# Optimization experiments

Hardware: AMD Instinct MI355X
Metric: run time of the kernel (lower is better)

Reference implementation:

```python
import jax, jax.numpy as jnp
import numpy as np

B, Q, K, D, H = 2, 2048, 2048, 1024, 16
HD = D // H  # 64
EPS = 1e-6  # flax LayerNorm default epsilon


def setup_inputs() -> dict:
    key = jax.random.key(0)
    ks = jax.random.split(key, 12)
    s = 1.0 / np.sqrt(D)  # lecun_normal-like scale
    inputs_q = jax.random.normal(ks[0], (B, Q, D), jnp.float32)
    bias = jax.random.normal(ks[1], (B, 1, Q, K), jnp.float32)
    mask = jax.random.randint(ks[2], (B, 1, Q, K), 0, 2).astype(jnp.bool_)
    wq = jax.random.normal(ks[3], (D, H, HD), jnp.float32) * s
    wk = jax.random.normal(ks[4], (D, H, HD), jnp.float32) * s
    wv = jax.random.normal(ks[5], (D, H, HD), jnp.float32) * s
    bq = jnp.zeros((H, HD), jnp.float32)
    bk = jnp.zeros((H, HD), jnp.float32)
    bv = jnp.zeros((H, HD), jnp.float32)
    q_scale = jnp.ones((HD,), jnp.float32)
    k_scale = jnp.ones((HD,), jnp.float32)
    wo = jax.random.normal(ks[6], (H, HD, D), jnp.float32) * s
    bo = jnp.zeros((D,), jnp.float32)
    return dict(inputs_q=inputs_q, bias=bias, mask=mask, wq=wq, bq=bq,
                wk=wk, bk=bk, wv=wv, bv=bv, q_scale=q_scale, k_scale=k_scale,
                wo=wo, bo=bo)


def _layernorm_nobias(x, scale):
    # normalize over last axis (head_dim), no bias, like flax LayerNorm(use_bias=False)
    mean = jnp.mean(x, axis=-1, keepdims=True)
    var = jnp.mean(jnp.square(x - mean), axis=-1, keepdims=True)
    return (x - mean) * jax.lax.rsqrt(var + EPS) * scale


def reference(inputs_q, bias, mask, wq, bq, wk, bk, wv, bv, q_scale, k_scale, wo, bo):
    # QKV projections (self-attention: k and v inputs default to inputs_q)
    q = jnp.einsum('bqd,dhe->bqhe', inputs_q, wq) + bq  # [B,Q,H,HD]
    k = jnp.einsum('bkd,dhe->bkhe', inputs_q, wk) + bk  # [B,K,H,HD]
    v = jnp.einsum('bkd,dhe->bkhe', inputs_q, wv) + bv  # [B,K,H,HD]
    # optional QK layernorm (normalize_qk=True)
    q = _layernorm_nobias(q, q_scale)
    k = _layernorm_nobias(k, k_scale)
    # attention weights
    q = q / jnp.sqrt(jnp.asarray(q.shape[-1], q.dtype))
    attn = jnp.einsum('bqhe,bkhe->bhqk', q, k)  # [B,H,Q,K]
    attn = attn + bias
    big_neg = jnp.finfo(q.dtype).min
    attn = jnp.where(mask, attn, big_neg)
    attn = jax.nn.softmax(attn.astype(jnp.float32), axis=-1).astype(q.dtype)
    # weighted values + output projection
    x = jnp.einsum('bhqk,bkhe->bqhe', attn, v)  # [B,Q,H,HD]
    out = jnp.einsum('bqhe,heo->bqo', x, wo) + bo  # [B,Q,D]
    return out
```

## Files before the change

kernel.cpp:

```cpp
#include <hip/hip_runtime.h>
#include <cstdint>
#include <cstddef>

typedef __bf16 bf16_t;
typedef __bf16 bf16x8 __attribute__((ext_vector_type(8)));
typedef float f32x4 __attribute__((ext_vector_type(4)));

constexpr int BB = 2, SS = 2048, DD = 1024, HH = 16, HDIM = 64;
constexpr int BS = BB * SS;
constexpr float LOG2E = 1.4426950408889634f;

__global__ void convert_x(const float* __restrict__ src, bf16_t* __restrict__ dst, int n4) {
  int i = blockIdx.x * blockDim.x + threadIdx.x;
  if (i >= n4) return;
  float4 v = ((const float4*)src)[i];
  union { bf16_t h[4]; uint2 u; } o;
  o.h[0] = (bf16_t)v.x; o.h[1] = (bf16_t)v.y; o.h[2] = (bf16_t)v.z; o.h[3] = (bf16_t)v.w;
  ((uint2*)dst)[i] = o.u;
}

__global__ void transpose_convert(const float* __restrict__ wq, const float* __restrict__ wk,
                                  const float* __restrict__ wv, const float* __restrict__ wo,
                                  bf16_t* __restrict__ wqkv_t, bf16_t* __restrict__ wo_t) {
  int which = blockIdx.z;
  const float* src = (which == 0) ? wq : (which == 1) ? wk : (which == 2) ? wv : wo;
  bf16_t* dst = (which < 3) ? wqkv_t : wo_t;
  int noff = (which < 3) ? which * 1024 : 0;
  __shared__ float tile[64][65];
  int tr = blockIdx.y, tc = blockIdx.x;
  int t = threadIdx.x;
#pragma unroll
  for (int p = 0; p < 4; ++p) {
    int e = (p * 256 + t) * 4;
    int r = e >> 6, c = e & 63;
    float4 v = *(const float4*)&src[(size_t)(tr * 64 + r) * 1024 + tc * 64 + c];
    tile[r][c] = v.x; tile[r][c + 1] = v.y; tile[r][c + 2] = v.z; tile[r][c + 3] = v.w;
  }
  __syncthreads();
#pragma unroll
  for (int p = 0; p < 4; ++p) {
    int e = (p * 256 + t) * 4;
    int r = e >> 6, c = e & 63;
    union { bf16_t h[4]; uint2 u; } o;
#pragma unroll
    for (int j = 0; j < 4; ++j) o.h[j] = (bf16_t)tile[c + j][r];
    *(uint2*)&dst[(size_t)(noff + tc * 64 + r) * 1024 + tr * 64 + c] = o.u;
  }
}

__global__ void prep_biasmask(const float* __restrict__ bias, const int* __restrict__ mask,
                              bf16_t* __restrict__ bmT) {
  __shared__ float tile[64][65];
  int qt = blockIdx.x, kt = blockIdx.y, b = blockIdx.z;
  int t = threadIdx.x;
  const size_t base = ((size_t)b * SS + qt * 64) * SS + kt * 64;
#pragma unroll
  for (int p = 0; p < 4; ++p) {
    int e = (p * 256 + t) * 4;
    int r = e >> 6, c = e & 63;
    float4 bv = *(const float4*)&bias[base + (size_t)r * SS + c];
    int4 mv = *(const int4*)&mask[base + (size_t)r * SS + c];
    tile[r][c]     = mv.x ? bv.x * LOG2E : -2.0e38f;
    tile[r][c + 1] = mv.y ? bv.y * LOG2E : -2.0e38f;
    tile[r][c + 2] = mv.z ? bv.z * LOG2E : -2.0e38f;
    tile[r][c + 3] = mv.w ? bv.w * LOG2E : -2.0e38f;
  }
  __syncthreads();
  const size_t obase = ((size_t)b * SS + kt * 64) * SS + qt * 64;
#pragma unroll
  for (int p = 0; p < 2; ++p) {
    int e = (p * 256 + t) * 8;
    int r = e >> 6, c = e & 63;
    union { bf16_t h[8]; uint4 u; } o;
#pragma unroll
    for (int j = 0; j < 8; ++j) o.h[j] = (bf16_t)tile[c + j][r];
    *(uint4*)&bmT[obase + (size_t)r * SS + c] = o.u;
  }
}

__global__ void vt_relayout(const bf16_t* __restrict__ Cqkv, const float* __restrict__ bv,
                            bf16_t* __restrict__ vt) {
  __shared__ float tile[64][65];
  int st = blockIdx.x, h = blockIdx.y, b = blockIdx.z;
  int t = threadIdx.x;
#pragma unroll
  for (int p = 0; p < 2; ++p) {
    int e = (p * 256 + t) * 8;
    int r = e >> 6, c = e & 63;
    bf16x8 v8 = *(const bf16x8*)&Cqkv[(size_t)(b * SS + st * 64 + r) * 3072 + 2048 + h * 64 + c];
#pragma unroll
    for (int j = 0; j < 8; ++j) tile[r][c + j] = (float)v8[j] + bv[h * 64 + c + j];
  }
  __syncthreads();
#pragma unroll
  for (int p = 0; p < 2; ++p) {
    int e = (p * 256 + t) * 8;
    int r = e >> 6, c = e & 63;
    union { bf16_t h[8]; uint4 u; } o;
#pragma unroll
    for (int j = 0; j < 8; ++j) o.h[j] = (bf16_t)tile[c + j][r];
    *(uint4*)&vt[(size_t)((b * HH + h) * HDIM + r) * SS + st * 64 + c] = o.u;
  }
}

template <bool OUT_F32>
__global__ __launch_bounds__(256) void gemm_bt(const bf16_t* __restrict__ A,
                                               const bf16_t* __restrict__ Bt,
                                               bf16_t* __restrict__ Cb, float* __restrict__ Cf,
                                               const float* __restrict__ bias, int M, int N,
                                               int Kd) {
  __shared__ __align__(16) bf16_t As[128][72];
  __shared__ __align__(16) bf16_t Bs[128][72];
  int tid = threadIdx.x;
  int lane = tid & 63, w = tid >> 6;
  int lo = lane & 15, quad = lane >> 4;
  int wm = w >> 1, wn = w & 1;
  int m0 = blockIdx.y * 128, n0 = blockIdx.x * 128;
  f32x4 acc[4][4] = {};
  for (int kk = 0; kk < Kd; kk += 64) {
#pragma unroll
    for (int p = 0; p < 4; ++p) {
      int idx = (p * 256 + tid) * 8;
      int r = idx >> 6, c = idx & 63;
      *(bf16x8*)&As[r][c] = *(const bf16x8*)&A[(size_t)(m0 + r) * Kd + kk + c];
      *(bf16x8*)&Bs[r][c] = *(const bf16x8*)&Bt[(size_t)(n0 + r) * Kd + kk + c];
    }
    __syncthreads();
#pragma unroll
    for (int kc = 0; kc < 2; ++kc) {
      bf16x8 am[4], bn[4];
#pragma unroll
      for (int i = 0; i < 4; ++i)
        am[i] = *(const bf16x8*)&As[wm * 64 + i * 16 + lo][kc * 32 + quad * 8];
#pragma unroll
      for (int i = 0; i < 4; ++i)
        bn[i] = *(const bf16x8*)&Bs[wn * 64 + i * 16 + lo][kc * 32 + quad * 8];
#pragma unroll
      for (int mi = 0; mi < 4; ++mi)
#pragma unroll
        for (int ni = 0; ni < 4; ++ni)
          acc[mi][ni] = __builtin_amdgcn_mfma_f32_16x16x32_bf16(am[mi], bn[ni], acc[mi][ni], 0, 0, 0);
    }
    __syncthreads();
  }
#pragma unroll
  for (int mi = 0; mi < 4; ++mi) {
#pragma unroll
    for (int ni = 0; ni < 4; ++ni) {
#pragma unroll
      for (int r = 0; r < 4; ++r) {
        int row = m0 + wm * 64 + mi * 16 + quad * 4 + r;
        int col = n0 + wn * 64 + ni * 16 + lo;
        float v = acc[mi][ni][r];
        if (OUT_F32)
          Cf[(size_t)row * N + col] = v + bias[col];
        else
          Cb[(size_t)row * N + col] = (bf16_t)v;
      }
    }
  }
}

__global__ void ln_relayout(const bf16_t* __restrict__ Cqkv, const float* __restrict__ bq,
                            const float* __restrict__ bk, const float* __restrict__ q_scale,
                            const float* __restrict__ k_scale, bf16_t* __restrict__ qb,
                            bf16_t* __restrict__ kb) {
  int mode = blockIdx.y;
  int vec = blockIdx.x * 4 + (threadIdx.x >> 6);
  int lane = threadIdx.x & 63;
  int bs = vec >> 4, h = vec & 15;
  int b = bs >> 11, s = bs & 2047;
  const float* badd = (mode == 0) ? bq : bk;
  float x = (float)Cqkv[(size_t)bs * 3072 + mode * 1024 + h * 64 + lane] + badd[h * 64 + lane];
  float sum = x;
#pragma unroll
  for (int off = 32; off >= 1; off >>= 1) sum += __shfl_xor(sum, off, 64);
  float mean = sum * (1.0f / 64.0f);
  float d = x - mean;
  float vs = d * d;
#pragma unroll
  for (int off = 32; off >= 1; off >>= 1) vs += __shfl_xor(vs, off, 64);
  float var = vs * (1.0f / 64.0f);
  const float* sc = (mode == 0) ? q_scale : k_scale;
  float y = d * rsqrtf(var + 1e-6f) * sc[lane];
  if (mode == 0) y *= 0.125f * LOG2E;
  bf16_t* dst = (mode == 0) ? qb : kb;
  dst[(size_t)((b * 16 + h) * 2048 + s) * 64 + lane] = (bf16_t)y;
}

__global__ __launch_bounds__(256) void attn_kernel(const bf16_t* __restrict__ qb,
                                                   const bf16_t* __restrict__ kb,
                                                   const bf16_t* __restrict__ vt,
                                                   const bf16_t* __restrict__ bmT,
                                                   bf16_t* __restrict__ xout) {
  __shared__ __align__(16) bf16_t Ks[64][72];
  __shared__ __align__(16) bf16_t Vs[64][72];
  __shared__ __align__(16) bf16_t Bm[64][72];
  __shared__ __align__(16) bf16_t Ps[4][16][72];
  int tid = threadIdx.x;
  int lane = tid & 63, w = tid >> 6;
  int lo = lane & 15, quad = lane >> 4;
  int qt = blockIdx.x, h = blockIdx.y, b = blockIdx.z;
  size_t headoff = (size_t)(b * HH + h) * SS * HDIM;
  const bf16_t* vthead = vt + headoff;
  const bf16_t* bmb = bmT + (size_t)b * SS * SS;

  const bf16_t* qptr = qb + headoff + (size_t)(qt * 64 + w * 16 + lo) * HDIM;
  bf16x8 aq0 = *(const bf16x8*)(qptr + quad * 8);
  bf16x8 aq1 = *(const bf16x8*)(qptr + 32 + quad * 8);

  bf16x8 ones;
#pragma unroll
  for (int j = 0; j < 8; ++j) ones[j] = (bf16_t)1.0f;

  f32x4 o[4] = {};
  f32x4 lacc = {};

  for (int kt = 0; kt < SS / 64; ++kt) {
#pragma unroll
    for (int p = 0; p < 2; ++p) {
      int idx = (p * 256 + tid) * 8;
      int r = idx >> 6, c = idx & 63;
      *(bf16x8*)&Ks[r][c] = *(const bf16x8*)&kb[headoff + (size_t)(kt * 64 + r) * HDIM + c];
      *(bf16x8*)&Vs[r][c] = *(const bf16x8*)&vthead[(size_t)r * SS + kt * 64 + c];
      *(bf16x8*)&Bm[r][c] = *(const bf16x8*)&bmb[(size_t)(kt * 64 + r) * SS + qt * 64 + c];
    }
    __syncthreads();

    f32x4 sc[4];
#pragma unroll
    for (int c = 0; c < 4; ++c) {
      union { bf16_t h[4]; uint2 u; } bm4;
      bm4.u = *(const uint2*)&Bm[c * 16 + lo][w * 16 + quad * 4];
#pragma unroll
      for (int r = 0; r < 4; ++r) sc[c][r] = (float)bm4.h[r];
      bf16x8 bk0 = *(const bf16x8*)&Ks[c * 16 + lo][quad * 8];
      bf16x8 bk1 = *(const bf16x8*)&Ks[c * 16 + lo][32 + quad * 8];
      sc[c] = __builtin_amdgcn_mfma_f32_16x16x32_bf16(aq0, bk0, sc[c], 0, 0, 0);
      sc[c] = __builtin_amdgcn_mfma_f32_16x16x32_bf16(aq1, bk1, sc[c], 0, 0, 0);
    }
#pragma unroll
    for (int c = 0; c < 4; ++c)
#pragma unroll
      for (int r = 0; r < 4; ++r)
        Ps[w][quad * 4 + r][c * 16 + lo] = (bf16_t)__builtin_amdgcn_exp2f(sc[c][r]);
    asm volatile("s_waitcnt lgkmcnt(0)" ::: "memory");
    bf16x8 ap0 = *(const bf16x8*)&Ps[w][lo][quad * 8];
    bf16x8 ap1 = *(const bf16x8*)&Ps[w][lo][32 + quad * 8];
    lacc = __builtin_amdgcn_mfma_f32_16x16x32_bf16(ap0, ones, lacc, 0, 0, 0);
    lacc = __builtin_amdgcn_mfma_f32_16x16x32_bf16(ap1, ones, lacc, 0, 0, 0);
#pragma unroll
    for (int t2 = 0; t2 < 4; ++t2) {
      bf16x8 bv0 = *(const bf16x8*)&Vs[t2 * 16 + lo][quad * 8];
      bf16x8 bv1 = *(const bf16x8*)&Vs[t2 * 16 + lo][32 + quad * 8];
      o[t2] = __builtin_amdgcn_mfma_f32_16x16x32_bf16(ap0, bv0, o[t2], 0, 0, 0);
      o[t2] = __builtin_amdgcn_mfma_f32_16x16x32_bf16(ap1, bv1, o[t2], 0, 0, 0);
    }
    __syncthreads();
  }
  float rl[4];
#pragma unroll
  for (int r = 0; r < 4; ++r) rl[r] = 1.0f / lacc[r];
#pragma unroll
  for (int t2 = 0; t2 < 4; ++t2) {
#pragma unroll
    for (int r = 0; r < 4; ++r) {
      int qa = qt * 64 + w * 16 + quad * 4 + r;
      xout[(size_t)(b * SS + qa) * DD + h * 64 + t2 * 16 + lo] = (bf16_t)(o[t2][r] * rl[r]);
    }
  }
}

extern "C" void kernel_launch(void* const* d_in, const int* in_sizes, int n_in, void* d_out,
                              int out_size, void* d_ws, size_t ws_size, hipStream_t stream) {
  const float* inputs_q = (const float*)d_in[0];
  const float* bias = (const float*)d_in[1];
  const int* mask = (const int*)d_in[2];
  const float* wq = (const float*)d_in[3];
  const float* bq = (const float*)d_in[4];
  const float* wk = (const float*)d_in[5];
  const float* bk = (const float*)d_in[6];
  const float* wv = (const float*)d_in[7];
  const float* bv = (const float*)d_in[8];
  const float* q_scale = (const float*)d_in[9];
  const float* k_scale = (const float*)d_in[10];
  const float* wo = (const float*)d_in[11];
  const float* bo = (const float*)d_in[12];
  float* out = (float*)d_out;

  char* ws = (char*)d_ws;
  bf16_t* xb     = (bf16_t*)(ws);
  bf16_t* wqkv_t = (bf16_t*)(ws + ((size_t)8 << 20));
  bf16_t* wo_t   = (bf16_t*)(ws + ((size_t)14 << 20));
  bf16_t* cqkv   = (bf16_t*)(ws + ((size_t)16 << 20));
  bf16_t* bmT    = (bf16_t*)(ws + ((size_t)16 << 20));
  bf16_t* qb2    = (bf16_t*)(ws + ((size_t)40 << 20));
  bf16_t* kb2    = (bf16_t*)(ws + ((size_t)48 << 20));
  bf16_t* vt     = (bf16_t*)(ws + ((size_t)56 << 20));
  bf16_t* xattn  = (bf16_t*)(ws + ((size_t)64 << 20));

  convert_x<<<(BS * DD / 4 + 255) / 256, 256, 0, stream>>>(inputs_q, xb, BS * DD / 4);
  transpose_convert<<<dim3(16, 16, 4), 256, 0, stream>>>(wq, wk, wv, wo, wqkv_t, wo_t);
  gemm_bt<false><<<dim3(24, 32), 256, 0, stream>>>(xb, wqkv_t, cqkv, nullptr, nullptr, BS, 3072, DD);
  ln_relayout<<<dim3(BS * HH / 4, 2), 256, 0, stream>>>(cqkv, bq, bk, q_scale, k_scale, qb2, kb2);
  vt_relayout<<<dim3(32, 16, 2), 256, 0, stream>>>(cqkv, bv, vt);
  prep_biasmask<<<dim3(32, 32, 2), 256, 0, stream>>>(bias, mask, bmT);
  attn_kernel<<<dim3(SS / 64, HH, BB), 256, 0, stream>>>(qb2, kb2, vt, bmT, xattn);
  gemm_bt<true><<<dim3(8, 32), 256, 0, stream>>>(xattn, wo_t, nullptr, out, bo, BS, 1024, DD);
}
```

Before: 333.9 us.

## Restructure attention to register-resident S^T tiles with f16 PV and untransposed bias

The attention kernel drops all shared-memory staging and block barriers. It computes S^T = K·Q^T directly in registers so the MFMA output layout can feed the P·V MFMA (16x16x16 f16) without a trip through LDS. Each wave now handles 32 queries instead of 16, which halves the grid and reuses each K and V fragment across two query groups. Bias/mask prep becomes a plain elementwise conversion in row-major order with a fixed -8 offset in the exponent to keep P inside f16 range, and V is stored as f16. The trade-offs are that K, V and bias are read straight from global/L2 with no cooperative tiling, and the constant -8 shift assumes logits stay bounded.

New measurement: 489.6 us. +46.6%, slower.

```diff
diff --git a/kernel.cpp b/kernel.cpp
--- a/kernel.cpp
+++ b/kernel.cpp
@@ -4,6 +4,9 @@
 
 typedef __bf16 bf16_t;
 typedef __bf16 bf16x8 __attribute__((ext_vector_type(8)));
+typedef __bf16 bf16x4 __attribute__((ext_vector_type(4)));
+typedef _Float16 f16_t;
+typedef _Float16 f16x4 __attribute__((ext_vector_type(4)));
 typedef float f32x4 __attribute__((ext_vector_type(4)));
 
 constexpr int BB = 2, SS = 2048, DD = 1024, HH = 16, HDIM = 64;
@@ -49,37 +52,26 @@
 }
 
 __global__ void prep_biasmask(const float* __restrict__ bias, const int* __restrict__ mask,
-                              bf16_t* __restrict__ bmT) {
-  __shared__ float tile[64][65];
-  int qt = blockIdx.x, kt = blockIdx.y, b = blockIdx.z;
-  int t = threadIdx.x;
-  const size_t base = ((size_t)b * SS + qt * 64) * SS + kt * 64;
-#pragma unroll
-  for (int p = 0; p < 4; ++p) {
-    int e = (p * 256 + t) * 4;
-    int r = e >> 6, c = e & 63;
-    float4 bv = *(const float4*)&bias[base + (size_t)r * SS + c];
-    int4 mv = *(const int4*)&mask[base + (size_t)r * SS + c];
-    tile[r][c]     = mv.x ? bv.x * LOG2E : -2.0e38f;
-    tile[r][c + 1] = mv.y ? bv.y * LOG2E : -2.0e38f;
-    tile[r][c + 2] = mv.z ? bv.z * LOG2E : -2.0e38f;
-    tile[r][c + 3] = mv.w ? bv.w * LOG2E : -2.0e38f;
-  }
-  __syncthreads();
-  const size_t obase = ((size_t)b * SS + kt * 64) * SS + qt * 64;
-#pragma unroll
-  for (int p = 0; p < 2; ++p) {
-    int e = (p * 256 + t) * 8;
-    int r = e >> 6, c = e & 63;
-    union { bf16_t h[8]; uint4 u; } o;
-#pragma unroll
-    for (int j = 0; j < 8; ++j) o.h[j] = (bf16_t)tile[c + j][r];
-    *(uint4*)&bmT[obase + (size_t)r * SS + c] = o.u;
-  }
+                              bf16_t* __restrict__ bmq) {
+  int i = blockIdx.x * blockDim.x + threadIdx.x;
+  float4 b0 = ((const float4*)bias)[i * 2];
+  float4 b1 = ((const float4*)bias)[i * 2 + 1];
+  int4 m0 = ((const int4*)mask)[i * 2];
+  int4 m1 = ((const int4*)mask)[i * 2 + 1];
+  union { bf16_t h[8]; uint4 u; } o;
+  o.h[0] = (bf16_t)(m0.x ? b0.x * LOG2E - 8.0f : -2.0e38f);
+  o.h[1] = (bf16_t)(m0.y ? b0.y * LOG2E - 8.0f : -2.0e38f);
+  o.h[2] = (bf16_t)(m0.z ? b0.z * LOG2E - 8.0f : -2.0e38f);
+  o.h[3] = (bf16_t)(m0.w ? b0.w * LOG2E - 8.0f : -2.0e38f);
+  o.h[4] = (bf16_t)(m1.x ? b1.x * LOG2E - 8.0f : -2.0e38f);
+  o.h[5] = (bf16_t)(m1.y ? b1.y * LOG2E - 8.0f : -2.0e38f);
+  o.h[6] = (bf16_t)(m1.z ? b1.z * LOG2E - 8.0f : -2.0e38f);
+  o.h[7] = (bf16_t)(m1.w ? b1.w * LOG2E - 8.0f : -2.0e38f);
+  ((uint4*)bmq)[i] = o.u;
 }
 
 __global__ void vt_relayout(const bf16_t* __restrict__ Cqkv, const float* __restrict__ bv,
-                            bf16_t* __restrict__ vt) {
+                            f16_t* __restrict__ vt) {
   __shared__ float tile[64][65];
   int st = blockIdx.x, h = blockIdx.y, b = blockIdx.z;
   int t = threadIdx.x;
@@ -96,9 +88,9 @@
   for (int p = 0; p < 2; ++p) {
     int e = (p * 256 + t) * 8;
     int r = e >> 6, c = e & 63;
-    union { bf16_t h[8]; uint4 u; } o;
-#pragma unroll
-    for (int j = 0; j < 8; ++j) o.h[j] = (bf16_t)tile[c + j][r];
+    union { f16_t h[8]; uint4 u; } o;
+#pragma unroll
+    for (int j = 0; j < 8; ++j) o.h[j] = (f16_t)tile[c + j][r];
     *(uint4*)&vt[(size_t)((b * HH + h) * HDIM + r) * SS + st * 64 + c] = o.u;
   }
 }
@@ -190,83 +182,88 @@
 
 __global__ __launch_bounds__(256) void attn_kernel(const bf16_t* __restrict__ qb,
                                                    const bf16_t* __restrict__ kb,
-                                                   const bf16_t* __restrict__ vt,
-                                                   const bf16_t* __restrict__ bmT,
+                                                   const f16_t* __restrict__ vt,
+                                                   const bf16_t* __restrict__ bmq,
                                                    bf16_t* __restrict__ xout) {
-  __shared__ __align__(16) bf16_t Ks[64][72];
-  __shared__ __align__(16) bf16_t Vs[64][72];
-  __shared__ __align__(16) bf16_t Bm[64][72];
-  __shared__ __align__(16) bf16_t Ps[4][16][72];
   int tid = threadIdx.x;
   int lane = tid & 63, w = tid >> 6;
   int lo = lane & 15, quad = lane >> 4;
   int qt = blockIdx.x, h = blockIdx.y, b = blockIdx.z;
   size_t headoff = (size_t)(b * HH + h) * SS * HDIM;
-  const bf16_t* vthead = vt + headoff;
-  const bf16_t* bmb = bmT + (size_t)b * SS * SS;
-
-  const bf16_t* qptr = qb + headoff + (size_t)(qt * 64 + w * 16 + lo) * HDIM;
-  bf16x8 aq0 = *(const bf16x8*)(qptr + quad * 8);
-  bf16x8 aq1 = *(const bf16x8*)(qptr + 32 + quad * 8);
-
-  bf16x8 ones;
-#pragma unroll
-  for (int j = 0; j < 8; ++j) ones[j] = (bf16_t)1.0f;
-
-  f32x4 o[4] = {};
-  f32x4 lacc = {};
+  int q0 = qt * 128 + w * 32;
+
+  const bf16_t* kbase = kb + headoff;
+  const f16_t* vbase = vt + headoff;
+
+  bf16x8 bqf[2][2];
+#pragma unroll
+  for (int qg = 0; qg < 2; ++qg)
+#pragma unroll
+    for (int ec = 0; ec < 2; ++ec)
+      bqf[qg][ec] =
+          *(const bf16x8*)&qb[headoff + (size_t)(q0 + qg * 16 + lo) * HDIM + ec * 32 + quad * 8];
+
+  const bf16_t* bmrow[2];
+#pragma unroll
+  for (int qg = 0; qg < 2; ++qg)
+    bmrow[qg] = bmq + (size_t)(b * SS + q0 + qg * 16 + lo) * SS;
+
+  f16x4 ones;
+#pragma unroll
+  for (int j = 0; j < 4; ++j) ones[j] = (f16_t)1.0f;
+
+  f32x4 ot[2][4] = {};
+  f32x4 lacc[2] = {};
 
   for (int kt = 0; kt < SS / 64; ++kt) {
-#pragma unroll
-    for (int p = 0; p < 2; ++p) {
-      int idx = (p * 256 + tid) * 8;
-      int r = idx >> 6, c = idx & 63;
-      *(bf16x8*)&Ks[r][c] = *(const bf16x8*)&kb[headoff + (size_t)(kt * 64 + r) * HDIM + c];
-      *(bf16x8*)&Vs[r][c] = *(const bf16x8*)&vthead[(size_t)r * SS + kt * 64 + c];
-      *(bf16x8*)&Bm[r][c] = *(const bf16x8*)&bmb[(size_t)(kt * 64 + r) * SS + qt * 64 + c];
-    }
-    __syncthreads();
-
-    f32x4 sc[4];
-#pragma unroll
-    for (int c = 0; c < 4; ++c) {
-      union { bf16_t h[4]; uint2 u; } bm4;
-      bm4.u = *(const uint2*)&Bm[c * 16 + lo][w * 16 + quad * 4];
-#pragma unroll
-      for (int r = 0; r < 4; ++r) sc[c][r] = (float)bm4.h[r];
-      bf16x8 bk0 = *(const bf16x8*)&Ks[c * 16 + lo][quad * 8];
-      bf16x8 bk1 = *(const bf16x8*)&Ks[c * 16 + lo][32 + quad * 8];
-      sc[c] = __builtin_amdgcn_mfma_f32_16x16x32_bf16(aq0, bk0, sc[c], 0, 0, 0);
-      sc[c] = __builtin_amdgcn_mfma_f32_16x16x32_bf16(aq1, bk1, sc[c], 0, 0, 0);
-    }
-#pragma unroll
-    for (int c = 0; c < 4; ++c)
-#pragma unroll
-      for (int r = 0; r < 4; ++r)
-        Ps[w][quad * 4 + r][c * 16 + lo] = (bf16_t)__builtin_amdgcn_exp2f(sc[c][r]);
-    asm volatile("s_waitcnt lgkmcnt(0)" ::: "memory");
-    bf16x8 ap0 = *(const bf16x8*)&Ps[w][lo][quad * 8];
-    bf16x8 ap1 = *(const bf16x8*)&Ps[w][lo][32 + quad * 8];
-    lacc = __builtin_amdgcn_mfma_f32_16x16x32_bf16(ap0, ones, lacc, 0, 0, 0);
-    lacc = __builtin_amdgcn_mfma_f32_16x16x32_bf16(ap1, ones, lacc, 0, 0, 0);
-#pragma unroll
-    for (int t2 = 0; t2 < 4; ++t2) {
-      bf16x8 bv0 = *(const bf16x8*)&Vs[t2 * 16 + lo][quad * 8];
-      bf16x8 bv1 = *(const bf16x8*)&Vs[t2 * 16 + lo][32 + quad * 8];
-      o[t2] = __builtin_amdgcn_mfma_f32_16x16x32_bf16(ap0, bv0, o[t2], 0, 0, 0);
-      o[t2] = __builtin_amdgcn_mfma_f32_16x16x32_bf16(ap1, bv1, o[t2], 0, 0, 0);
-    }
-    __syncthreads();
-  }
-  float rl[4];
-#pragma unroll
-  for (int r = 0; r < 4; ++r) rl[r] = 1.0f / lacc[r];
-#pragma unroll
-  for (int t2 = 0; t2 < 4; ++t2) {
-#pragma unroll
-    for (int r = 0; r < 4; ++r) {
-      int qa = qt * 64 + w * 16 + quad * 4 + r;
-      xout[(size_t)(b * SS + qa) * DD + h * 64 + t2 * 16 + lo] = (bf16_t)(o[t2][r] * rl[r]);
+    int k0 = kt * 64;
+    bf16x8 ka[4][2];
+#pragma unroll
+    for (int mb = 0; mb < 4; ++mb)
+#pragma unroll
+      for (int ec = 0; ec < 2; ++ec)
+        ka[mb][ec] =
+            *(const bf16x8*)&kbase[(size_t)(k0 + mb * 16 + lo) * HDIM + ec * 32 + quad * 8];
+
+    f16x4 pf[2][4];
+#pragma unroll
+    for (int qg = 0; qg < 2; ++qg) {
+#pragma unroll
+      for (int mb = 0; mb < 4; ++mb) {
+        bf16x4 bm4 = *(const bf16x4*)&bmrow[qg][k0 + mb * 16 + quad * 4];
+        f32x4 s;
+#pragma unroll
+        for (int r = 0; r < 4; ++r) s[r] = (float)bm4[r];
+        s = __builtin_amdgcn_mfma_f32_16x16x32_bf16(ka[mb][0], bqf[qg][0], s, 0, 0, 0);
+        s = __builtin_amdgcn_mfma_f32_16x16x32_bf16(ka[mb][1], bqf[qg][1], s, 0, 0, 0);
+#pragma unroll
+        for (int r = 0; r < 4; ++r) pf[qg][mb][r] = (f16_t)__builtin_amdgcn_exp2f(s[r]);
+      }
+    }
+#pragma unroll
+    for (int mb = 0; mb < 4; ++mb) {
+#pragma unroll
+      for (int eb = 0; eb < 4; ++eb) {
+        f16x4 va = *(const f16x4*)&vbase[(size_t)(eb * 16 + lo) * SS + k0 + mb * 16 + quad * 4];
+#pragma unroll
+        for (int qg = 0; qg < 2; ++qg)
+          ot[qg][eb] = __builtin_amdgcn_mfma_f32_16x16x16f16(va, pf[qg][mb], ot[qg][eb], 0, 0, 0);
+      }
+#pragma unroll
+      for (int qg = 0; qg < 2; ++qg)
+        lacc[qg] = __builtin_amdgcn_mfma_f32_16x16x16f16(ones, pf[qg][mb], lacc[qg], 0, 0, 0);
+    }
+  }
+#pragma unroll
+  for (int qg = 0; qg < 2; ++qg) {
+    float rl = 1.0f / lacc[qg][0];
+    int q = q0 + qg * 16 + lo;
+#pragma unroll
+    for (int eb = 0; eb < 4; ++eb) {
+      union { bf16_t h4[4]; uint2 u; } o;
+#pragma unroll
+      for (int r = 0; r < 4; ++r) o.h4[r] = (bf16_t)(ot[qg][eb][r] * rl);
+      *(uint2*)&xout[(size_t)(b * SS + q) * DD + h * 64 + eb * 16 + quad * 4] = o.u;
     }
   }
 }
@@ -293,18 +290,18 @@
   bf16_t* wqkv_t = (bf16_t*)(ws + ((size_t)8 << 20));
   bf16_t* wo_t   = (bf16_t*)(ws + ((size_t)14 << 20));
   bf16_t* cqkv   = (bf16_t*)(ws + ((size_t)16 << 20));
-  bf16_t* bmT    = (bf16_t*)(ws + ((size_t)16 << 20));
+  bf16_t* bmq    = (bf16_t*)(ws + ((size_t)16 << 20));
   bf16_t* qb2    = (bf16_t*)(ws + ((size_t)40 << 20));
   bf16_t* kb2    = (bf16_t*)(ws + ((size_t)48 << 20));
-  bf16_t* vt     = (bf16_t*)(ws + ((size_t)56 << 20));
+  f16_t*  vtb    = (f16_t*)(ws + ((size_t)56 << 20));
   bf16_t* xattn  = (bf16_t*)(ws + ((size_t)64 << 20));
 
   convert_x<<<(BS * DD / 4 + 255) / 256, 256, 0, stream>>>(inputs_q, xb, BS * DD / 4);
   transpose_convert<<<dim3(16, 16, 4), 256, 0, stream>>>(wq, wk, wv, wo, wqkv_t, wo_t);
   gemm_bt<false><<<dim3(24, 32), 256, 0, stream>>>(xb, wqkv_t, cqkv, nullptr, nullptr, BS, 3072, DD);
   ln_relayout<<<dim3(BS * HH / 4, 2), 256, 0, stream>>>(cqkv, bq, bk, q_scale, k_scale, qb2, kb2);
-  vt_relayout<<<dim3(32, 16, 2), 256, 0, stream>>>(cqkv, bv, vt);
-  prep_biasmask<<<dim3(32, 32, 2), 256, 0, stream>>>(bias, mask, bmT);
-  attn_kernel<<<dim3(SS / 64, HH, BB), 256, 0, stream>>>(qb2, kb2, vt, bmT, xattn);
+  vt_relayout<<<dim3(32, 16, 2), 256, 0, stream>>>(cqkv, bv, vtb);
+  prep_biasmask<<<BB * SS * SS / 8 / 256, 256, 0, stream>>>(bias, mask, bmq);
+  attn_kernel<<<dim3(SS / 128, HH, BB), 256, 0, stream>>>(qb2, kb2, vtb, bmq, xattn);
   gemm_bt<true><<<dim3(8, 32), 256, 0, stream>>>(xattn, wo_t, nullptr, out, bo, BS, 1024, DD);
 }
```
